# Performance work log

Hardware: AMD Instinct MI355X
Metric: run time of the kernel (lower is better)

## Reference

```python
import jax, jax.numpy as jnp
import numpy as np

B, T, D, E = 2, 1653, 512, 8
D_E = D // E
BE = B * E


def setup_inputs() -> dict:
    key = jax.random.key(0)
    ks = jax.random.split(key, 11)
    s = 0.02  # keep linear-layer scale sane
    return {
        "input": jax.random.normal(ks[0], (B, T, D), jnp.float32),
        "Wq": jax.random.normal(ks[1], (D, D), jnp.float32) * s,
        "bq": jax.random.normal(ks[2], (D,), jnp.float32) * s,
        "Wk": jax.random.normal(ks[3], (D, D), jnp.float32) * s,
        "bk": jax.random.normal(ks[4], (D,), jnp.float32) * s,
        "Wv": jax.random.normal(ks[5], (D, D), jnp.float32) * s,
        "bv": jax.random.normal(ks[6], (D,), jnp.float32) * s,
        "Wo": jax.random.normal(ks[7], (D, D), jnp.float32) * s,
        "bo": jax.random.normal(ks[8], (D,), jnp.float32) * s,
        # random 'gaussian orthogonal punishment' matrix (diag(norms) @ blockwise-QR in torch; random here)
        "punish": jax.random.normal(ks[9], (T, T), jnp.float32) * (1.0 / np.sqrt(T)),
        # random tensor produced by torch.nn.init.orthogonal_(att_score) in the source
        "att_orth": jax.random.normal(ks[10], (BE, T, T), jnp.float32) * (1.0 / np.sqrt(T)),
    }


def _learnable_sigmoid(x):
    return 1.2 / (1.0 + jnp.exp(-1.6 * x))


def reference(input, Wq, bq, Wk, bk, Wv, bv, Wo, bo, punish, att_orth):
    # torch nn.Linear: y = x @ W^T + b
    def proj(W, b):
        # [B,T,D] -> permute(0,2,1) -> [B,D,T] -> reshape to [B*E, T, D_E]
        y = jnp.einsum('btd,ed->bte', input, W) + b
        return y.transpose(0, 2, 1).reshape(BE, T, D_E)

    Q = _learnable_sigmoid(proj(Wq, bq))            # [BE, T, D_E] (mask_q is all-ones => no-op)
    K = _learnable_sigmoid(proj(Wk, bk))            # [BE, T, D_E]
    V = proj(Wv, bv)                                # [BE, T, D_E]

    inv_sqrt_T = 1.0 / jnp.sqrt(jnp.float32(T))
    att = jnp.einsum('btd,bsd->bts', Q, K) * inv_sqrt_T  # [BE, T, T]

    # punishment: elementwise mul by broadcast punish matrix, then matmul with
    # the (transposed) random orthogonal tensor: att = (att * P) @ orth^T
    att = (att * punish[None, :, :]) @ att_orth.transpose(0, 2, 1)  # [BE, T, T]

    att = jnp.where(att == 0.0, jnp.float32(-2e20), att)  # masked_fill(att==0, -2e20)

    out = jnp.einsum('bts,bsd->btd', att, V)        # [BE, T, D_E]
    # permute(0,2,1) -> [BE, D_E, T] -> reshape [B, D, T] -> permute -> [B, T, D]
    out = out.transpose(0, 2, 1).reshape(B, D, T).transpose(0, 2, 1)
    return jnp.einsum('btd,ed->bte', out, Wo) + bo   # [B, T, D]
```

## Files before the change

kernel.cpp:

```cpp
#include <hip/hip_runtime.h>

#define TT 1653
#define DD 512
#define BB 2
#define DE 64
#define BEH 16
#define TTILES 26
#define TPAD 1664
#define SQN 26
#define NJC 4
#define MPSTRIDE TPAD

typedef __attribute__((ext_vector_type(8))) short bf16x8;
typedef __attribute__((ext_vector_type(4))) float f32x4;
typedef float f32x4u  __attribute__((ext_vector_type(4), aligned(4)));

__device__ __forceinline__ short f2bf(float f) {
    union { float f; unsigned u; } v; v.f = f;
    unsigned r = v.u + 0x7fffu + ((v.u >> 16) & 1u);
    return (short)(r >> 16);
}
__device__ __forceinline__ unsigned pack2(float a, float b) {
    return (unsigned)(unsigned short)f2bf(a) | ((unsigned)(unsigned short)f2bf(b) << 16);
}
__device__ __forceinline__ float bf2f(short s) {
    union { unsigned u; float f; } v; v.u = ((unsigned)(unsigned short)s) << 16;
    return v.f;
}

__device__ __forceinline__ void bar_fenced() {
    __builtin_amdgcn_sched_barrier(0);
    __builtin_amdgcn_s_barrier();
    __builtin_amdgcn_sched_barrier(0);
}
__device__ __forceinline__ void lgkm0_bar() {
    asm volatile("s_waitcnt lgkmcnt(0)" ::: "memory");
    __builtin_amdgcn_sched_barrier(0);
    __builtin_amdgcn_s_barrier();
    __builtin_amdgcn_sched_barrier(0);
}

__global__ __launch_bounds__(256) void convp2_kernel(
    const float* __restrict__ P, short* __restrict__ Pbf)
{
    const int g = blockIdx.x * 256 + threadIdx.x;
    const int NG4 = TPAD / 4;
    if (g >= TT * NG4) return;
    const int r = g / NG4, c4 = (g - r * NG4) * 4;
    float p0 = 0.f, p1 = 0.f, p2 = 0.f, p3 = 0.f;
    const float* prow = P + (size_t)r * TT;
    if (c4 + 0 < TT) p0 = prow[c4 + 0];
    if (c4 + 1 < TT) p1 = prow[c4 + 1];
    if (c4 + 2 < TT) p2 = prow[c4 + 2];
    if (c4 + 3 < TT) p3 = prow[c4 + 3];
    uint2 o; o.x = pack2(p0, p1); o.y = pack2(p2, p3);
    *(uint2*)(Pbf + (size_t)r * TPAD + c4) = o;
}

__global__ __launch_bounds__(256) void proj4_kernel(
    const float* __restrict__ X,
    const float* __restrict__ W0, const float* __restrict__ b0,
    const float* __restrict__ W1, const float* __restrict__ b1,
    const float* __restrict__ W2, const float* __restrict__ b2,
    short* __restrict__ Y0, short* __restrict__ Y1, short* __restrict__ Y2)
{
    __shared__ __align__(16) short Wsh[64][72];
    __shared__ __align__(16) short Xs[64][72];

    const int tt = blockIdx.x, dt = blockIdx.y, z = blockIdx.z;
    const int b = z / 3, which = z % 3;
    const float* W    = (which == 0) ? W0 : (which == 1) ? W1 : W2;
    const float* bias = (which == 0) ? b0 : (which == 1) ? b1 : b2;
    short* Y          = (which == 0) ? Y0 : (which == 1) ? Y1 : Y2;

    const int t0 = tt * 64, d0 = dt * 64;
    const float* Xb = X + (size_t)b * TT * DD;

    const int tid  = threadIdx.x;
    const int wave = tid >> 6, lane = tid & 63;
    const int quad = lane >> 4, l16 = lane & 15;
    const int srow = tid >> 2, scg = (tid & 3) * 16;
    const int trow = t0 + srow;
    const int rx = min(trow, TT - 1);

    f32x4 acc[4];
    #pragma unroll
    for (int i = 0; i < 4; ++i) acc[i] = (f32x4){0.f, 0.f, 0.f, 0.f};

    float4 w0, w1, w2, w3, x0, x1, x2, x3;

    auto stage = [&](int k0) {
        const float* wrow = W + (size_t)(d0 + srow) * DD + k0 + scg;
        w0 = *(const float4*)(wrow);
        w1 = *(const float4*)(wrow + 4);
        w2 = *(const float4*)(wrow + 8);
        w3 = *(const float4*)(wrow + 12);
        const float* xrow = Xb + (size_t)rx * DD + k0 + scg;
        x0 = *(const float4*)(xrow);
        x1 = *(const float4*)(xrow + 4);
        x2 = *(const float4*)(xrow + 8);
        x3 = *(const float4*)(xrow + 12);
    };
    auto lds_write = [&]() {
        const bool tv = (trow < TT);
        float4 zz = make_float4(0.f, 0.f, 0.f, 0.f);
        float4 y0 = tv ? x0 : zz, y1 = tv ? x1 : zz;
        float4 y2 = tv ? x2 : zz, y3 = tv ? x3 : zz;
        uint4 pw0, pw1, px0, px1;
        pw0.x = pack2(w0.x, w0.y); pw0.y = pack2(w0.z, w0.w);
        pw0.z = pack2(w1.x, w1.y); pw0.w = pack2(w1.z, w1.w);
        pw1.x = pack2(w2.x, w2.y); pw1.y = pack2(w2.z, w2.w);
        pw1.z = pack2(w3.x, w3.y); pw1.w = pack2(w3.z, w3.w);
        px0.x = pack2(y0.x, y0.y); px0.y = pack2(y0.z, y0.w);
        px0.z = pack2(y1.x, y1.y); px0.w = pack2(y1.z, y1.w);
        px1.x = pack2(y2.x, y2.y); px1.y = pack2(y2.z, y2.w);
        px1.z = pack2(y3.x, y3.y); px1.w = pack2(y3.z, y3.w);
        *(uint4*)&Wsh[srow][scg]     = pw0;
        *(uint4*)&Wsh[srow][scg + 8] = pw1;
        *(uint4*)&Xs[srow][scg]      = px0;
        *(uint4*)&Xs[srow][scg + 8]  = px1;
    };

    stage(0);
    for (int k0 = 0; k0 < DD; k0 += 64) {
        lds_write();
        if (k0 + 64 < DD) stage(k0 + 64);
        lgkm0_bar();

        #pragma unroll
        for (int ks = 0; ks < 2; ++ks) {
            bf16x8 a = *(const bf16x8*)&Wsh[wave * 16 + l16][ks * 32 + quad * 8];
            #pragma unroll
            for (int nt = 0; nt < 4; ++nt) {
                bf16x8 bb = *(const bf16x8*)&Xs[nt * 16 + l16][ks * 32 + quad * 8];
                acc[nt] = __builtin_amdgcn_mfma_f32_16x16x32_bf16(a, bb, acc[nt], 0, 0, 0);
            }
        }
        bar_fenced();
    }

    #pragma unroll
    for (int nt = 0; nt < 4; ++nt) {
        const int t = t0 + nt * 16 + l16;
        if (t < TT) {
            #pragma unroll
            for (int r = 0; r < 4; ++r) {
                const int d = d0 + wave * 16 + quad * 4 + r;
                float v = acc[nt][r] + bias[d];
                if (which < 2) v = 1.2f / (1.0f + __expf(-1.6f * v));
                Y[((size_t)b * DD + d) * TT + t] = f2bf(v);
            }
        }
    }
}

struct OVStage {
    f32x4u o0a, o0b, o1a, o1b;
    uint2  v0a, v0b, v1a, v1b;
};

__global__ __launch_bounds__(256) void ovt6_kernel(
    const float* __restrict__ orth, const short* __restrict__ Vb,
    float* __restrict__ Mpart)
{
    __shared__ __align__(16) short Os[64][72];
    __shared__ __align__(16) short Vs[64][72];

    const int sq = blockIdx.x, be = blockIdx.y, jc = blockIdx.z;
    const int s0 = sq * 64;
    const int jt0 = (jc < 2) ? jc * 7 : 14 + (jc - 2) * 6;
    const int jtn = (jc < 2) ? 7 : 6;

    const float* O  = orth + (size_t)be * TT * TT;
    const short* Vh = Vb + (size_t)be * DE * TT;

    const int tid  = threadIdx.x;
    const int wave = tid >> 6, lane = tid & 63;
    const int quad = lane >> 4, l16 = lane & 15;

    const int p  = tid & 15;
    const int sc = tid >> 4;
    const int ca = s0 + 4 * sc;
    const bool fastS = (s0 + 64 <= TT);

    f32x4 acc[4];
    #pragma unroll
    for (int i = 0; i < 4; ++i) acc[i] = (f32x4){0.f, 0.f, 0.f, 0.f};

    auto stage_load = [&](OVStage& S, int j0) {
        const int jA = j0 + 2 * p;
        const int r0  = min(jA,      TT - 1);
        const int r0b = min(jA + 1,  TT - 1);
        const int r1  = min(jA + 32, TT - 1);
        const int r1b = min(jA + 33, TT - 1);
        if (fastS) {
            S.o0a = *(const f32x4u*)(O + (size_t)r0  * TT + ca);
            S.o0b = *(const f32x4u*)(O + (size_t)r0b * TT + ca);
            S.o1a = *(const f32x4u*)(O + (size_t)r1  * TT + ca);
            S.o1b = *(const f32x4u*)(O + (size_t)r1b * TT + ca);
        } else {
            #pragma unroll
            for (int i = 0; i < 4; ++i) {
                const int col = ca + i;
                const bool cv = (col < TT);
                S.o0a[i] = cv ? O[(size_t)r0  * TT + col] : 0.f;
                S.o0b[i] = cv ? O[(size_t)r0b * TT + col] : 0.f;
                S.o1a[i] = cv ? O[(size_t)r1  * TT + col] : 0.f;
                S.o1b[i] = cv ? O[(size_t)r1b * TT + col] : 0.f;
            }
        }
        S.v0a = *(const uint2*)(Vh + (size_t)r0  * DE + 4 * sc);
        S.v0b = *(const uint2*)(Vh + (size_t)r0b * DE + 4 * sc);
        S.v1a = *(const uint2*)(Vh + (size_t)r1  * DE + 4 * sc);
        S.v1b = *(const uint2*)(Vh + (size_t)r1b * DE + 4 * sc);
    };

    auto lds_write = [&](const OVStage& S, int j0) {
        const int jA = j0 + 2 * p;
        #pragma unroll
        for (int i = 0; i < 4; ++i) {
            *(unsigned*)&Os[4 * sc + i][2 * p]      = pack2(S.o0a[i], S.o0b[i]);
            *(unsigned*)&Os[4 * sc + i][2 * p + 32] = pack2(S.o1a[i], S.o1b[i]);
        }
        const uint2 z = make_uint2(0u, 0u);
        uint2 v0a = (jA      < TT) ? S.v0a : z;
        uint2 v0b = (jA + 1  < TT) ? S.v0b : z;
        uint2 v1a = (jA + 32 < TT) ? S.v1a : z;
        uint2 v1b = (jA + 33 < TT) ? S.v1b : z;
        *(unsigned*)&Vs[4 * sc + 0][2 * p]      = (v0a.x & 0xffffu) | (v0b.x << 16);
        *(unsigned*)&Vs[4 * sc + 1][2 * p]      = (v0a.x >> 16)     | (v0b.x & 0xffff0000u);
        *(unsigned*)&Vs[4 * sc + 2][2 * p]      = (v0a.y & 0xffffu) | (v0b.y << 16);
        *(unsigned*)&Vs[4 * sc + 3][2 * p]      = (v0a.y >> 16)     | (v0b.y & 0xffff0000u);
        *(unsigned*)&Vs[4 * sc + 0][2 * p + 32] = (v1a.x & 0xffffu) | (v1b.x << 16);
        *(unsigned*)&Vs[4 * sc + 1][2 * p + 32] = (v1a.x >> 16)     | (v1b.x & 0xffff0000u);
        *(unsigned*)&Vs[4 * sc + 2][2 * p + 32] = (v1a.y & 0xffffu) | (v1b.y << 16);
        *(unsigned*)&Vs[4 * sc + 3][2 * p + 32] = (v1a.y >> 16)     | (v1b.y & 0xffff0000u);
    };

    auto mfma_tile = [&]() {
        #pragma unroll
        for (int ks = 0; ks < 2; ++ks) {
            bf16x8 bb = *(const bf16x8*)&Os[wave * 16 + l16][ks * 32 + quad * 8];
            #pragma unroll
            for (int i = 0; i < 4; ++i) {
                bf16x8 a = *(const bf16x8*)&Vs[i * 16 + l16][ks * 32 + quad * 8];
                acc[i] = __builtin_amdgcn_mfma_f32_16x16x32_bf16(a, bb, acc[i], 0, 0, 0);
            }
        }
    };

    OVStage sA, sB;
    stage_load(sA, (jt0 + 0) * 64);
    stage_load(sB, (jt0 + 1) * 64);

    for (int t = 0; t < jtn; t += 2) {
        lds_write(sA, (jt0 + t) * 64);
        if (t + 2 < jtn) stage_load(sA, (jt0 + t + 2) * 64);
        lgkm0_bar();
        mfma_tile();
        bar_fenced();
        if (t + 1 < jtn) {
            lds_write(sB, (jt0 + t + 1) * 64);
            if (t + 3 < jtn) stage_load(sB, (jt0 + t + 3) * 64);
            lgkm0_bar();
            mfma_tile();
            bar_fenced();
        }
    }

    float* Mp = Mpart + (size_t)(jc * BEH + be) * DE * MPSTRIDE;
    const int s = s0 + wave * 16 + l16;
    #pragma unroll
    for (int i = 0; i < 4; ++i) {
        #pragma unroll
        for (int r = 0; r < 4; ++r) {
            const int d = i * 16 + quad * 4 + r;
            Mp[(size_t)d * MPSTRIDE + s] = acc[i][r];
        }
    }
}

__global__ __launch_bounds__(256) void mreduce_kernel(
    const float* __restrict__ Mpart, short* __restrict__ Mt)
{
    const int g = blockIdx.x * 256 + threadIdx.x;
    const int NG = TPAD / 4;
    if (g >= BEH * DE * NG) return;
    const int bd = g / NG;
    const int s4 = (g - bd * NG) * 4;

    const size_t jstride = (size_t)BEH * DE * MPSTRIDE;
    const float* p = Mpart + (size_t)bd * MPSTRIDE + s4;
    float4 a0 = *(const float4*)(p);
    float4 a1 = *(const float4*)(p + jstride);
    float4 a2 = *(const float4*)(p + 2 * jstride);
    float4 a3 = *(const float4*)(p + 3 * jstride);
    float s0 = a0.x + a1.x + a2.x + a3.x;
    float s1 = a0.y + a1.y + a2.y + a3.y;
    float s2 = a0.z + a1.z + a2.z + a3.z;
    float s3 = a0.w + a1.w + a2.w + a3.w;

    uint2 o;
    o.x = pack2(s0, s1);
    o.y = pack2(s2, s3);
    *(uint2*)(Mt + (size_t)bd * TPAD + s4) = o;
}

struct AStage {
    uint4 k0, k1, m0, m1, p0, p1;
};

__global__ __launch_bounds__(256) void attn4_kernel(
    const short* __restrict__ Qb, const short* __restrict__ Kb,
    const short* __restrict__ Mt, const short* __restrict__ Pbf,
    float* __restrict__ Hbuf)
{
    __shared__ __align__(16) short Qs[64][72];
    __shared__ __align__(16) short Ks[64][72];
    __shared__ __align__(16) short Ms[64][72];
    __shared__ __align__(16) short Ps[64][72];

    const int it = blockIdx.x, be = blockIdx.y;
    const int b = be >> 3, e = be & 7;
    const int i0 = it * 64;
    const short* Qh = Qb + (size_t)be * DE * TT;
    const short* Kh = Kb + (size_t)be * DE * TT;
    const short* Mh = Mt + (size_t)be * DE * TPAD;

    const int tid  = threadIdx.x;
    const int wave = tid >> 6, lane = tid & 63;
    const int quad = lane >> 4, l16 = lane & 15;

    const float invs = 0.024598297f;

    const int srow = tid >> 2, scg = (tid & 3) * 16;
    const int gi = i0 + srow;
    const bool giv = (gi < TT);
    const int ri = min(gi, TT - 1);

    {
        uint4 z = make_uint4(0u, 0u, 0u, 0u);
        uint4 v0 = *(const uint4*)(Qh + (size_t)ri * DE + scg);
        uint4 v1 = *(const uint4*)(Qh + (size_t)ri * DE + scg + 8);
        if (!giv) { v0 = z; v1 = z; }
        *(uint4*)&Qs[srow][scg]     = v0;
        *(uint4*)&Qs[srow][scg + 8] = v1;
    }

    f32x4 out[4];
    #pragma unroll
    for (int i = 0; i < 4; ++i) out[i] = (f32x4){0.f, 0.f, 0.f, 0.f};

    auto stage_regs = [&](AStage& S, int s0) {
        const int gs = s0 + srow;
        const int rs = min(gs, TT - 1);
        S.k0 = *(const uint4*)(Kh + (size_t)rs * DE + scg);
        S.k1 = *(const uint4*)(Kh + (size_t)rs * DE + scg + 8);
        S.m0 = *(const uint4*)(Mh + (size_t)srow * TPAD + s0 + scg);
        S.m1 = *(const uint4*)(Mh + (size_t)srow * TPAD + s0 + scg + 8);
        S.p0 = *(const uint4*)(Pbf + (size_t)ri * TPAD + s0 + scg);
        S.p1 = *(const uint4*)(Pbf + (size_t)ri * TPAD + s0 + scg + 8);
    };

    auto lds_write = [&](const AStage& S, int s0) {
        const int gs = s0 + srow;
        const uint4 z = make_uint4(0u, 0u, 0u, 0u);
        const bool kv = (gs < TT);
        uint4 k0 = kv ? S.k0 : z, k1 = kv ? S.k1 : z;
        uint4 p0 = giv ? S.p0 : z, p1 = giv ? S.p1 : z;
        *(uint4*)&Ks[srow][scg]     = k0;
        *(uint4*)&Ks[srow][scg + 8] = k1;
        *(uint4*)&Ms[srow][scg]     = S.m0;
        *(uint4*)&Ms[srow][scg + 8] = S.m1;
        *(uint4*)&Ps[srow][scg]     = p0;
        *(uint4*)&Ps[srow][scg + 8] = p1;
    };

    auto compute = [&]() {
        f32x4 w[4];
        #pragma unroll
        for (int i = 0; i < 4; ++i) w[i] = (f32x4){0.f, 0.f, 0.f, 0.f};
        #pragma unroll
        for (int ks = 0; ks < 2; ++ks) {
            bf16x8 a = *(const bf16x8*)&Qs[wave * 16 + l16][ks * 32 + quad * 8];
            #pragma unroll
            for (int stile = 0; stile < 4; ++stile) {
                bf16x8 bb = *(const bf16x8*)&Ks[stile * 16 + l16][ks * 32 + quad * 8];
                w[stile] = __builtin_amdgcn_mfma_f32_16x16x32_bf16(a, bb, w[stile], 0, 0, 0);
            }
        }

        #pragma unroll
        for (int stile = 0; stile < 4; ++stile) {
            const int sl = stile * 16 + l16;
            #pragma unroll
            for (int r = 0; r < 4; ++r) {
                const int il = wave * 16 + quad * 4 + r;
                float v = w[stile][r] * invs * bf2f(Ps[il][sl]);
                Ps[il][sl] = f2bf(v);
            }
        }

        #pragma unroll
        for (int ks = 0; ks < 2; ++ks) {
            bf16x8 a = *(const bf16x8*)&Ps[wave * 16 + l16][ks * 32 + quad * 8];
            #pragma unroll
            for (int dt = 0; dt < 4; ++dt) {
                bf16x8 bb = *(const bf16x8*)&Ms[dt * 16 + l16][ks * 32 + quad * 8];
                out[dt] = __builtin_amdgcn_mfma_f32_16x16x32_bf16(a, bb, out[dt], 0, 0, 0);
            }
        }
    };

    AStage sA, sB;
    stage_regs(sA, 0);
    stage_regs(sB, 64);
    lgkm0_bar();

    for (int tt = 0; tt < TTILES; tt += 2) {
        lds_write(sA, tt * 64);
        if (tt + 2 < TTILES) stage_regs(sA, (tt + 2) * 64);
        lgkm0_bar();
        compute();
        bar_fenced();
        lds_write(sB, (tt + 1) * 64);
        if (tt + 3 < TTILES) stage_regs(sB, (tt + 3) * 64);
        lgkm0_bar();
        compute();
        bar_fenced();
    }

    #pragma unroll
    for (int dt = 0; dt < 4; ++dt) {
        const int d = dt * 16 + l16;
        #pragma unroll
        for (int r = 0; r < 4; ++r) {
            const int go = i0 + wave * 16 + quad * 4 + r;
            if (go < TT)
                Hbuf[((size_t)b * TT + go) * DD + e * 64 + d] = out[dt][r];
        }
    }
}

__global__ __launch_bounds__(256) void oproj_kernel(
    const float* __restrict__ H, const float* __restrict__ Wo,
    const float* __restrict__ bo, float* __restrict__ out)
{
    __shared__ float Hs[16][68];
    __shared__ float Ns[16][68];

    const int tt = blockIdx.x, nt = blockIdx.y, b = blockIdx.z;
    const int t0 = tt * 64, n0 = nt * 64;
    const float* Hb = H + (size_t)b * TT * DD;

    const int tid = threadIdx.x;
    const int tx = tid & 15, ty = tid >> 4;
    const int lrow = tid >> 2, lq = tid & 3;
    const int trow = t0 + lrow;

    float acc[4][4] = {};

    for (int k0 = 0; k0 < DD; k0 += 16) {
        float4 hv = make_float4(0.f, 0.f, 0.f, 0.f);
        if (trow < TT)
            hv = *(const float4*)(Hb + (size_t)trow * DD + k0 + lq*4);
        float4 wv = *(const float4*)(Wo + (size_t)(n0 + lrow) * DD + k0 + lq*4);
        __syncthreads();
        Hs[lq*4+0][lrow] = hv.x; Hs[lq*4+1][lrow] = hv.y;
        Hs[lq*4+2][lrow] = hv.z; Hs[lq*4+3][lrow] = hv.w;
        Ns[lq*4+0][lrow] = wv.x; Ns[lq*4+1][lrow] = wv.y;
        Ns[lq*4+2][lrow] = wv.z; Ns[lq*4+3][lrow] = wv.w;
        __syncthreads();
        #pragma unroll
        for (int k = 0; k < 16; ++k) {
            float4 a4 = *(const float4*)(&Hs[k][ty*4]);
            float4 c4 = *(const float4*)(&Ns[k][tx*4]);
            float a[4] = {a4.x, a4.y, a4.z, a4.w};
            float c[4] = {c4.x, c4.y, c4.z, c4.w};
            #pragma unroll
            for (int i = 0; i < 4; ++i)
                #pragma unroll
                for (int j = 0; j < 4; ++j)
                    acc[i][j] = fmaf(a[i], c[j], acc[i][j]);
        }
        __syncthreads();
    }

    #pragma unroll
    for (int i = 0; i < 4; ++i) {
        const int t = t0 + ty*4 + i;
        if (t < TT) {
            float4 v;
            v.x = acc[i][0] + bo[n0 + tx*4 + 0];
            v.y = acc[i][1] + bo[n0 + tx*4 + 1];
            v.z = acc[i][2] + bo[n0 + tx*4 + 2];
            v.w = acc[i][3] + bo[n0 + tx*4 + 3];
            *(float4*)(out + ((size_t)b * TT + t) * DD + n0 + tx*4) = v;
        }
    }
}

extern "C" void kernel_launch(void* const* d_in, const int* in_sizes, int n_in,
                              void* d_out, int out_size, void* d_ws, size_t ws_size,
                              hipStream_t stream)
{
    (void)in_sizes; (void)n_in; (void)out_size; (void)ws_size;

    const float* X    = (const float*)d_in[0];
    const float* Wq   = (const float*)d_in[1];
    const float* bq   = (const float*)d_in[2];
    const float* Wk   = (const float*)d_in[3];
    const float* bk   = (const float*)d_in[4];
    const float* Wv   = (const float*)d_in[5];
    const float* bv   = (const float*)d_in[6];
    const float* Wo   = (const float*)d_in[7];
    const float* bo   = (const float*)d_in[8];
    const float* P    = (const float*)d_in[9];
    const float* orth = (const float*)d_in[10];
    float* out = (float*)d_out;

    char* ws = (char*)d_ws;
    const size_t SZH = (size_t)BB * DD * TT * sizeof(short);
    short* Qb  = (short*)(ws);
    short* Kb  = (short*)(ws + SZH);
    short* Vb  = (short*)(ws + 2 * SZH);
    short* Mtb = (short*)(ws + 3 * SZH);
    short* Pbf = (short*)(ws + 3 * SZH + (size_t)BEH * DE * TPAD * sizeof(short));
    char*  after_p = ws + 3 * SZH + (size_t)BEH * DE * TPAD * sizeof(short)
                        + (size_t)TT * TPAD * sizeof(short);
    float* Mpart = (float*)after_p;
    float* Hbuf  = (float*)after_p;

    dim3 blk(256);

    convp2_kernel<<<dim3((TT * (TPAD / 4) + 255) / 256), blk, 0, stream>>>(P, Pbf);

    dim3 g1(TTILES, DD / 64, BB * 3);
    proj4_kernel<<<g1, blk, 0, stream>>>(X, Wq, bq, Wk, bk, Wv, bv, Qb, Kb, Vb);

    dim3 g2(SQN, BEH, NJC);
    ovt6_kernel<<<g2, blk, 0, stream>>>(orth, Vb, Mpart);

    dim3 gr((BEH * DE * (TPAD / 4) + 255) / 256);
    mreduce_kernel<<<gr, blk, 0, stream>>>(Mpart, Mtb);

    dim3 g3(TTILES, BEH);
    attn4_kernel<<<g3, blk, 0, stream>>>(Qb, Kb, Mtb, Pbf, Hbuf);

    dim3 g4(TTILES, DD / 64, BB);
    oproj_kernel<<<g4, blk, 0, stream>>>(Hbuf, Wo, bo, out);
}
```

Before: 406.5 us.

## Split attention and output projection along K, add reduce kernels, double-buffer staging

The attention kernel gains a third grid dimension that splits the key/sequence tiles into four chunks, each writing partial head outputs that a new reduce kernel sums. The output projection is split-K in two halves with register double-buffering, and a final reduce adds the halves and the bias. The orth·V kernel is split into eight j-chunks instead of four, and the QKV projection gets two-stage register prefetching. The goal is to raise grid occupancy on the large CU count, at the cost of extra partial-buffer traffic, more workspace and extra launches.

```diff
diff --git a/kernel.cpp b/kernel.cpp
--- a/kernel.cpp
+++ b/kernel.cpp
@@ -8,8 +8,10 @@
 #define TTILES 26
 #define TPAD 1664
 #define SQN 26
-#define NJC 4
+#define NJC 8
+#define SCN 4
 #define MPSTRIDE TPAD
+#define HSTRIDE ((size_t)BB * TT * DD)
 
 typedef __attribute__((ext_vector_type(8))) short bf16x8;
 typedef __attribute__((ext_vector_type(4))) float f32x4;
@@ -57,7 +59,9 @@
     *(uint2*)(Pbf + (size_t)r * TPAD + c4) = o;
 }
 
-__global__ __launch_bounds__(256) void proj4_kernel(
+struct PStage { float4 w0, w1, w2, w3, x0, x1, x2, x3; };
+
+__global__ __launch_bounds__(256) void proj5_kernel(
     const float* __restrict__ X,
     const float* __restrict__ W0, const float* __restrict__ b0,
     const float* __restrict__ W1, const float* __restrict__ b1,
@@ -87,30 +91,28 @@
     #pragma unroll
     for (int i = 0; i < 4; ++i) acc[i] = (f32x4){0.f, 0.f, 0.f, 0.f};
 
-    float4 w0, w1, w2, w3, x0, x1, x2, x3;
-
-    auto stage = [&](int k0) {
+    auto stage = [&](PStage& S, int k0) {
         const float* wrow = W + (size_t)(d0 + srow) * DD + k0 + scg;
-        w0 = *(const float4*)(wrow);
-        w1 = *(const float4*)(wrow + 4);
-        w2 = *(const float4*)(wrow + 8);
-        w3 = *(const float4*)(wrow + 12);
+        S.w0 = *(const float4*)(wrow);
+        S.w1 = *(const float4*)(wrow + 4);
+        S.w2 = *(const float4*)(wrow + 8);
+        S.w3 = *(const float4*)(wrow + 12);
         const float* xrow = Xb + (size_t)rx * DD + k0 + scg;
-        x0 = *(const float4*)(xrow);
-        x1 = *(const float4*)(xrow + 4);
-        x2 = *(const float4*)(xrow + 8);
-        x3 = *(const float4*)(xrow + 12);
-    };
-    auto lds_write = [&]() {
+        S.x0 = *(const float4*)(xrow);
+        S.x1 = *(const float4*)(xrow + 4);
+        S.x2 = *(const float4*)(xrow + 8);
+        S.x3 = *(const float4*)(xrow + 12);
+    };
+    auto lds_write = [&](const PStage& S) {
         const bool tv = (trow < TT);
         float4 zz = make_float4(0.f, 0.f, 0.f, 0.f);
-        float4 y0 = tv ? x0 : zz, y1 = tv ? x1 : zz;
-        float4 y2 = tv ? x2 : zz, y3 = tv ? x3 : zz;
+        float4 y0 = tv ? S.x0 : zz, y1 = tv ? S.x1 : zz;
+        float4 y2 = tv ? S.x2 : zz, y3 = tv ? S.x3 : zz;
         uint4 pw0, pw1, px0, px1;
-        pw0.x = pack2(w0.x, w0.y); pw0.y = pack2(w0.z, w0.w);
-        pw0.z = pack2(w1.x, w1.y); pw0.w = pack2(w1.z, w1.w);
-        pw1.x = pack2(w2.x, w2.y); pw1.y = pack2(w2.z, w2.w);
-        pw1.z = pack2(w3.x, w3.y); pw1.w = pack2(w3.z, w3.w);
+        pw0.x = pack2(S.w0.x, S.w0.y); pw0.y = pack2(S.w0.z, S.w0.w);
+        pw0.z = pack2(S.w1.x, S.w1.y); pw0.w = pack2(S.w1.z, S.w1.w);
+        pw1.x = pack2(S.w2.x, S.w2.y); pw1.y = pack2(S.w2.z, S.w2.w);
+        pw1.z = pack2(S.w3.x, S.w3.y); pw1.w = pack2(S.w3.z, S.w3.w);
         px0.x = pack2(y0.x, y0.y); px0.y = pack2(y0.z, y0.w);
         px0.z = pack2(y1.x, y1.y); px0.w = pack2(y1.z, y1.w);
         px1.x = pack2(y2.x, y2.y); px1.y = pack2(y2.z, y2.w);
@@ -120,13 +122,7 @@
         *(uint4*)&Xs[srow][scg]      = px0;
         *(uint4*)&Xs[srow][scg + 8]  = px1;
     };
-
-    stage(0);
-    for (int k0 = 0; k0 < DD; k0 += 64) {
-        lds_write();
-        if (k0 + 64 < DD) stage(k0 + 64);
-        lgkm0_bar();
-
+    auto mfma_tile = [&]() {
         #pragma unroll
         for (int ks = 0; ks < 2; ++ks) {
             bf16x8 a = *(const bf16x8*)&Wsh[wave * 16 + l16][ks * 32 + quad * 8];
@@ -136,6 +132,21 @@
                 acc[nt] = __builtin_amdgcn_mfma_f32_16x16x32_bf16(a, bb, acc[nt], 0, 0, 0);
             }
         }
+    };
+
+    PStage sA, sB;
+    stage(sA, 0);
+    stage(sB, 64);
+    for (int k0 = 0; k0 < DD; k0 += 128) {
+        lds_write(sA);
+        if (k0 + 128 < DD) stage(sA, k0 + 128);
+        lgkm0_bar();
+        mfma_tile();
+        bar_fenced();
+        lds_write(sB);
+        if (k0 + 192 < DD) stage(sB, k0 + 192);
+        lgkm0_bar();
+        mfma_tile();
         bar_fenced();
     }
 
@@ -159,7 +170,7 @@
     uint2  v0a, v0b, v1a, v1b;
 };
 
-__global__ __launch_bounds__(256) void ovt6_kernel(
+__global__ __launch_bounds__(256) void ovt7_kernel(
     const float* __restrict__ orth, const short* __restrict__ Vb,
     float* __restrict__ Mpart)
 {
@@ -168,8 +179,8 @@
 
     const int sq = blockIdx.x, be = blockIdx.y, jc = blockIdx.z;
     const int s0 = sq * 64;
-    const int jt0 = (jc < 2) ? jc * 7 : 14 + (jc - 2) * 6;
-    const int jtn = (jc < 2) ? 7 : 6;
+    const int jt0 = (jc < 2) ? jc * 4 : 8 + (jc - 2) * 3;
+    const int jtn = (jc < 2) ? 4 : 3;
 
     const float* O  = orth + (size_t)be * TT * TT;
     const short* Vh = Vb + (size_t)be * DE * TT;
@@ -291,14 +302,12 @@
 
     const size_t jstride = (size_t)BEH * DE * MPSTRIDE;
     const float* p = Mpart + (size_t)bd * MPSTRIDE + s4;
-    float4 a0 = *(const float4*)(p);
-    float4 a1 = *(const float4*)(p + jstride);
-    float4 a2 = *(const float4*)(p + 2 * jstride);
-    float4 a3 = *(const float4*)(p + 3 * jstride);
-    float s0 = a0.x + a1.x + a2.x + a3.x;
-    float s1 = a0.y + a1.y + a2.y + a3.y;
-    float s2 = a0.z + a1.z + a2.z + a3.z;
-    float s3 = a0.w + a1.w + a2.w + a3.w;
+    float s0 = 0.f, s1 = 0.f, s2 = 0.f, s3 = 0.f;
+    #pragma unroll
+    for (int j = 0; j < NJC; ++j) {
+        float4 a = *(const float4*)(p + j * jstride);
+        s0 += a.x; s1 += a.y; s2 += a.z; s3 += a.w;
+    }
 
     uint2 o;
     o.x = pack2(s0, s1);
@@ -310,19 +319,22 @@
     uint4 k0, k1, m0, m1, p0, p1;
 };
 
-__global__ __launch_bounds__(256) void attn4_kernel(
+__global__ __launch_bounds__(256) void attn5_kernel(
     const short* __restrict__ Qb, const short* __restrict__ Kb,
     const short* __restrict__ Mt, const short* __restrict__ Pbf,
-    float* __restrict__ Hbuf)
+    float* __restrict__ Hpart)
 {
     __shared__ __align__(16) short Qs[64][72];
     __shared__ __align__(16) short Ks[64][72];
     __shared__ __align__(16) short Ms[64][72];
     __shared__ __align__(16) short Ps[64][72];
 
-    const int it = blockIdx.x, be = blockIdx.y;
+    const int it = blockIdx.x, be = blockIdx.y, sch = blockIdx.z;
     const int b = be >> 3, e = be & 7;
     const int i0 = it * 64;
+    const int st0 = (sch < 2) ? sch * 7 : 14 + (sch - 2) * 6;
+    const int stn = (sch < 2) ? 7 : 6;
+
     const short* Qh = Qb + (size_t)be * DE * TT;
     const short* Kh = Kb + (size_t)be * DE * TT;
     const short* Mh = Mt + (size_t)be * DE * TPAD;
@@ -389,7 +401,6 @@
                 w[stile] = __builtin_amdgcn_mfma_f32_16x16x32_bf16(a, bb, w[stile], 0, 0, 0);
             }
         }
-
         #pragma unroll
         for (int stile = 0; stile < 4; ++stile) {
             const int sl = stile * 16 + l16;
@@ -400,7 +411,6 @@
                 Ps[il][sl] = f2bf(v);
             }
         }
-
         #pragma unroll
         for (int ks = 0; ks < 2; ++ks) {
             bf16x8 a = *(const bf16x8*)&Ps[wave * 16 + l16][ks * 32 + quad * 8];
@@ -413,23 +423,26 @@
     };
 
     AStage sA, sB;
-    stage_regs(sA, 0);
-    stage_regs(sB, 64);
+    stage_regs(sA, (st0 + 0) * 64);
+    stage_regs(sB, (st0 + 1) * 64);
     lgkm0_bar();
 
-    for (int tt = 0; tt < TTILES; tt += 2) {
-        lds_write(sA, tt * 64);
-        if (tt + 2 < TTILES) stage_regs(sA, (tt + 2) * 64);
+    for (int t = 0; t < stn; t += 2) {
+        lds_write(sA, (st0 + t) * 64);
+        if (t + 2 < stn) stage_regs(sA, (st0 + t + 2) * 64);
         lgkm0_bar();
         compute();
         bar_fenced();
-        lds_write(sB, (tt + 1) * 64);
-        if (tt + 3 < TTILES) stage_regs(sB, (tt + 3) * 64);
-        lgkm0_bar();
-        compute();
-        bar_fenced();
-    }
-
+        if (t + 1 < stn) {
+            lds_write(sB, (st0 + t + 1) * 64);
+            if (t + 3 < stn) stage_regs(sB, (st0 + t + 3) * 64);
+            lgkm0_bar();
+            compute();
+            bar_fenced();
+        }
+    }
+
+    float* Hp = Hpart + (size_t)sch * HSTRIDE;
     #pragma unroll
     for (int dt = 0; dt < 4; ++dt) {
         const int d = dt * 16 + l16;
@@ -437,40 +450,65 @@
         for (int r = 0; r < 4; ++r) {
             const int go = i0 + wave * 16 + quad * 4 + r;
             if (go < TT)
-                Hbuf[((size_t)b * TT + go) * DD + e * 64 + d] = out[dt][r];
-        }
-    }
-}
-
-__global__ __launch_bounds__(256) void oproj_kernel(
+                Hp[((size_t)b * TT + go) * DD + e * 64 + d] = out[dt][r];
+        }
+    }
+}
+
+__global__ __launch_bounds__(256) void hreduce_kernel(
+    const float* __restrict__ Hpart, float* __restrict__ Hbuf)
+{
+    const int g = blockIdx.x * 256 + threadIdx.x;
+    const size_t n4 = HSTRIDE / 4;
+    if ((size_t)g >= n4) return;
+    const size_t off = (size_t)g * 4;
+    float4 a0 = *(const float4*)(Hpart + off);
+    float4 a1 = *(const float4*)(Hpart + HSTRIDE + off);
+    float4 a2 = *(const float4*)(Hpart + 2 * HSTRIDE + off);
+    float4 a3 = *(const float4*)(Hpart + 3 * HSTRIDE + off);
+    float4 o;
+    o.x = a0.x + a1.x + a2.x + a3.x;
+    o.y = a0.y + a1.y + a2.y + a3.y;
+    o.z = a0.z + a1.z + a2.z + a3.z;
+    o.w = a0.w + a1.w + a2.w + a3.w;
+    *(float4*)(Hbuf + off) = o;
+}
+
+struct OStage { float4 h, w; };
+
+__global__ __launch_bounds__(256) void oproj2_kernel(
     const float* __restrict__ H, const float* __restrict__ Wo,
-    const float* __restrict__ bo, float* __restrict__ out)
+    float* __restrict__ opart)
 {
     __shared__ float Hs[16][68];
     __shared__ float Ns[16][68];
 
-    const int tt = blockIdx.x, nt = blockIdx.y, b = blockIdx.z;
+    const int tt = blockIdx.x, nt = blockIdx.y, z = blockIdx.z;
+    const int b = z & 1, h = z >> 1;
     const int t0 = tt * 64, n0 = nt * 64;
+    const int kbase = h * 256;
     const float* Hb = H + (size_t)b * TT * DD;
 
     const int tid = threadIdx.x;
     const int tx = tid & 15, ty = tid >> 4;
     const int lrow = tid >> 2, lq = tid & 3;
     const int trow = t0 + lrow;
+    const int rx = min(trow, TT - 1);
 
     float acc[4][4] = {};
 
-    for (int k0 = 0; k0 < DD; k0 += 16) {
-        float4 hv = make_float4(0.f, 0.f, 0.f, 0.f);
-        if (trow < TT)
-            hv = *(const float4*)(Hb + (size_t)trow * DD + k0 + lq*4);
-        float4 wv = *(const float4*)(Wo + (size_t)(n0 + lrow) * DD + k0 + lq*4);
-        __syncthreads();
+    auto stage = [&](OStage& S, int k0) {
+        S.h = *(const float4*)(Hb + (size_t)rx * DD + k0 + lq * 4);
+        S.w = *(const float4*)(Wo + (size_t)(n0 + lrow) * DD + k0 + lq * 4);
+    };
+    auto lds_write = [&](const OStage& S) {
+        float4 hv = (trow < TT) ? S.h : make_float4(0.f, 0.f, 0.f, 0.f);
         Hs[lq*4+0][lrow] = hv.x; Hs[lq*4+1][lrow] = hv.y;
         Hs[lq*4+2][lrow] = hv.z; Hs[lq*4+3][lrow] = hv.w;
-        Ns[lq*4+0][lrow] = wv.x; Ns[lq*4+1][lrow] = wv.y;
-        Ns[lq*4+2][lrow] = wv.z; Ns[lq*4+3][lrow] = wv.w;
-        __syncthreads();
+        Ns[lq*4+0][lrow] = S.w.x; Ns[lq*4+1][lrow] = S.w.y;
+        Ns[lq*4+2][lrow] = S.w.z; Ns[lq*4+3][lrow] = S.w.w;
+    };
+    auto compute = [&]() {
         #pragma unroll
         for (int k = 0; k < 16; ++k) {
             float4 a4 = *(const float4*)(&Hs[k][ty*4]);
@@ -483,21 +521,54 @@
                 for (int j = 0; j < 4; ++j)
                     acc[i][j] = fmaf(a[i], c[j], acc[i][j]);
         }
-        __syncthreads();
-    }
-
+    };
+
+    OStage sA, sB;
+    stage(sA, kbase);
+    stage(sB, kbase + 16);
+    for (int k0 = 0; k0 < 256; k0 += 32) {
+        lds_write(sA);
+        if (k0 + 32 < 256) stage(sA, kbase + k0 + 32);
+        lgkm0_bar();
+        compute();
+        bar_fenced();
+        lds_write(sB);
+        if (k0 + 48 < 256) stage(sB, kbase + k0 + 48);
+        lgkm0_bar();
+        compute();
+        bar_fenced();
+    }
+
+    float* op = opart + (size_t)h * HSTRIDE;
     #pragma unroll
     for (int i = 0; i < 4; ++i) {
         const int t = t0 + ty*4 + i;
         if (t < TT) {
             float4 v;
-            v.x = acc[i][0] + bo[n0 + tx*4 + 0];
-            v.y = acc[i][1] + bo[n0 + tx*4 + 1];
-            v.z = acc[i][2] + bo[n0 + tx*4 + 2];
-            v.w = acc[i][3] + bo[n0 + tx*4 + 3];
-            *(float4*)(out + ((size_t)b * TT + t) * DD + n0 + tx*4) = v;
-        }
-    }
+            v.x = acc[i][0]; v.y = acc[i][1]; v.z = acc[i][2]; v.w = acc[i][3];
+            *(float4*)(op + ((size_t)b * TT + t) * DD + n0 + tx*4) = v;
+        }
+    }
+}
+
+__global__ __launch_bounds__(256) void oreduce_kernel(
+    const float* __restrict__ opart, const float* __restrict__ bo,
+    float* __restrict__ out)
+{
+    const int g = blockIdx.x * 256 + threadIdx.x;
+    const size_t n4 = HSTRIDE / 4;
+    if ((size_t)g >= n4) return;
+    const size_t off = (size_t)g * 4;
+    const int n0 = (int)(off % DD);
+    float4 a0 = *(const float4*)(opart + off);
+    float4 a1 = *(const float4*)(opart + HSTRIDE + off);
+    float4 bv = *(const float4*)(bo + n0);
+    float4 o;
+    o.x = a0.x + a1.x + bv.x;
+    o.y = a0.y + a1.y + bv.y;
+    o.z = a0.z + a1.z + bv.z;
+    o.w = a0.w + a1.w + bv.w;
+    *(float4*)(out + off) = o;
 }
 
 extern "C" void kernel_launch(void* const* d_in, const int* in_sizes, int n_in,
@@ -521,32 +592,41 @@
 
     char* ws = (char*)d_ws;
     const size_t SZH = (size_t)BB * DD * TT * sizeof(short);
+    const size_t SZMT = (size_t)BEH * DE * TPAD * sizeof(short);
+    const size_t SZP  = (size_t)TT * TPAD * sizeof(short);
     short* Qb  = (short*)(ws);
     short* Kb  = (short*)(ws + SZH);
     short* Vb  = (short*)(ws + 2 * SZH);
     short* Mtb = (short*)(ws + 3 * SZH);
-    short* Pbf = (short*)(ws + 3 * SZH + (size_t)BEH * DE * TPAD * sizeof(short));
-    char*  after_p = ws + 3 * SZH + (size_t)BEH * DE * TPAD * sizeof(short)
-                        + (size_t)TT * TPAD * sizeof(short);
-    float* Mpart = (float*)after_p;
-    float* Hbuf  = (float*)after_p;
+    short* Pbf = (short*)(ws + 3 * SZH + SZMT);
+    char*  base1 = ws + 3 * SZH + SZMT + SZP;
+    float* Hbuf  = (float*)base1;
+    float* opart = (float*)(base1 + HSTRIDE * sizeof(float));
+    char*  base2 = base1 + 3 * HSTRIDE * sizeof(float);
+    float* Mpart = (float*)base2;
+    float* Hpart = (float*)base2;
 
     dim3 blk(256);
 
     convp2_kernel<<<dim3((TT * (TPAD / 4) + 255) / 256), blk, 0, stream>>>(P, Pbf);
 
     dim3 g1(TTILES, DD / 64, BB * 3);
-    proj4_kernel<<<g1, blk, 0, stream>>>(X, Wq, bq, Wk, bk, Wv, bv, Qb, Kb, Vb);
+    proj5_kernel<<<g1, blk, 0, stream>>>(X, Wq, bq, Wk, bk, Wv, bv, Qb, Kb, Vb);
 
     dim3 g2(SQN, BEH, NJC);
-    ovt6_kernel<<<g2, blk, 0, stream>>>(orth, Vb, Mpart);
+    ovt7_kernel<<<g2, blk, 0, stream>>>(orth, Vb, Mpart);
 
     dim3 gr((BEH * DE * (TPAD / 4) + 255) / 256);
     mreduce_kernel<<<gr, blk, 0, stream>>>(Mpart, Mtb);
 
-    dim3 g3(TTILES, BEH);
-    attn4_kernel<<<g3, blk, 0, stream>>>(Qb, Kb, Mtb, Pbf, Hbuf);
-
-    dim3 g4(TTILES, DD / 64, BB);
-    oproj_kernel<<<g4, blk, 0, stream>>>(Hbuf, Wo, bo, out);
-}
+    dim3 g3(TTILES, BEH, SCN);
+    attn5_kernel<<<g3, blk, 0, stream>>>(Qb, Kb, Mtb, Pbf, Hpart);
+
+    dim3 gh((unsigned)((HSTRIDE / 4 + 255) / 256));
+    hreduce_kernel<<<gh, blk, 0, stream>>>(Hpart, Hbuf);
+
+    dim3 g4(TTILES, DD / 64, BB * 2);
+    oproj2_kernel<<<g4, blk, 0, stream>>>(Hbuf, Wo, opart);
+
+    oreduce_kernel<<<gh, blk, 0, stream>>>(opart, bo, out);
+}
```

New measurement: 416.0 us. +2.3%, slower.
